# Kernel tuning notes

Measured on AMD Instinct MI355X. Metric: run time of the kernel, lower is better.

## Reference

```python
import jax, jax.numpy as jnp
import numpy as np
from jax import lax

# pywt db4 filters (8 taps)
_DEC_LO = np.array([-0.010597401784997278, 0.032883011666982945, 0.030841381835986965,
                    -0.18703481171888114, -0.02798376941698385, 0.6308807679295904,
                    0.7148465705525415, 0.23037781330885523])
_DEC_HI = np.array([-0.23037781330885523, 0.7148465705525415, -0.6308807679295904,
                    -0.02798376941698385, 0.18703481171888114, 0.030841381835986965,
                    -0.032883011666982945, -0.010597401784997278])
_REC_LO = _DEC_LO[::-1].copy()
_REC_HI = _DEC_HI[::-1].copy()
_L = 8  # filter length
LEVELS = 4


def _dwt_level(x):
    # x: (M, n) -> (cA, cD) each (M, (n+_L-1)//2), pywt 'symmetric' mode
    xe = jnp.pad(x, ((0, 0), (_L - 1, _L - 1)), mode='symmetric')[:, 1:]
    ker = jnp.stack([_DEC_LO[::-1], _DEC_HI[::-1]]).astype(x.dtype)[:, None, :]  # (2,1,L)
    y = lax.conv_general_dilated(xe[:, None, :], ker, (2,), 'VALID')  # (M,2,m)
    return y[:, 0], y[:, 1]


def _idwt_level(ca, cd, out_len):
    # inverse DWT, cropped to out_len (matches length of next-finer approximation)
    inp = jnp.stack([ca, cd], axis=1)  # (M,2,m)
    ker = jnp.stack([_REC_LO[::-1], _REC_HI[::-1]]).astype(ca.dtype)[None]  # (1,2,L)
    y = lax.conv_general_dilated(inp, ker, (1,), [(_L - 1, _L - 1)], lhs_dilation=(2,))
    return y[:, 0, _L - 2:_L - 2 + out_len]


def setup_inputs() -> dict:
    key = jax.random.key(0)
    k1, k2, k3, k4 = jax.random.split(key, 4)
    B, N, C = 32, 8192, 64
    m = N
    for _ in range(LEVELS):
        m = (m + _L - 1) // 2  # 518
    scale = 1.0 / (C * C)
    return {
        'x': jax.random.normal(k1, (B, N, C), jnp.float32),
        'w1': scale * jax.random.uniform(k2, (C, C, m), jnp.float32),
        'w2': scale * jax.random.uniform(k3, (C, C, m), jnp.float32),
        'dense_kernel': jax.random.normal(k4, (C, C), jnp.float32) / jnp.sqrt(C).astype(jnp.float32),
        'dense_bias': jnp.zeros((C,), jnp.float32),
    }


def reference(x, w1, w2, dense_kernel, dense_bias):
    B, N, C = x.shape
    xc = jnp.transpose(x, (0, 2, 1)).reshape(B * C, N)  # per-(batch,channel) signals
    # analysis: multi-level DWT
    lens, details = [], []
    a = xc
    for _ in range(LEVELS):
        lens.append(a.shape[1])
        a, d = _dwt_level(a)
        details.append(d)
    m = a.shape[1]
    # channel mixing on coarsest approximation and coarsest detail (WNO kernel)
    a = jnp.einsum('bim,iom->bom', a.reshape(B, C, m), w1).reshape(B * C, m)
    details[-1] = jnp.einsum('bim,iom->bom', details[-1].reshape(B, C, m), w2).reshape(B * C, m)
    # synthesis: multi-level IDWT
    for j in range(LEVELS - 1, -1, -1):
        a = _idwt_level(a, details[j], lens[j])
    y = jnp.transpose(a.reshape(B, C, N), (0, 2, 1))
    shortcut = x @ dense_kernel + dense_bias  # Dense 1x1 shortcut
    out = y + shortcut
    return out * jnp.tanh(jax.nn.softplus(out))  # mish
```

## Files before the change

kernel.cpp:

```cpp
#include <hip/hip_runtime.h>
#include <hip/hip_bf16.h>
#include <stdint.h>

typedef __attribute__((ext_vector_type(8))) short short8;
typedef __attribute__((ext_vector_type(4))) float floatx4;

__device__ __constant__ float c_DL[8] = {
    -0.010597401784997278f, 0.032883011666982945f, 0.030841381835986965f,
    -0.18703481171888114f, -0.02798376941698385f, 0.6308807679295904f,
    0.7148465705525415f, 0.23037781330885523f};
__device__ __constant__ float c_DH[8] = {
    -0.23037781330885523f, 0.7148465705525415f, -0.6308807679295904f,
    -0.02798376941698385f, 0.18703481171888114f, 0.030841381835986965f,
    -0.032883011666982945f, -0.010597401784997278f};
__device__ __constant__ float c_RL[8] = {
    0.23037781330885523f, 0.7148465705525415f, 0.6308807679295904f,
    -0.02798376941698385f, -0.18703481171888114f, 0.030841381835986965f,
    0.032883011666982945f, -0.010597401784997278f};
__device__ __constant__ float c_RH[8] = {
    -0.010597401784997278f, -0.032883011666982945f, 0.030841381835986965f,
    0.18703481171888114f, -0.02798376941698385f, -0.6308807679295904f,
    0.7148465705525415f, -0.23037781330885523f};

__device__ __forceinline__ float bflo(uint32_t u) { return __uint_as_float(u << 16); }
__device__ __forceinline__ float bfhi(uint32_t u) { return __uint_as_float(u & 0xffff0000u); }
__device__ __forceinline__ float bfu(unsigned short u) { return __uint_as_float(((uint32_t)u) << 16); }
__device__ __forceinline__ short f2bs(float f) {
  __hip_bfloat16 h = __float2bfloat16(f);
  return *reinterpret_cast<short*>(&h);
}

__device__ __forceinline__ int reflect_idx(int t, int n) {
  if (t < 0) t = -1 - t;
  if (t >= n) t = 2 * n - 1 - t;
  return t;
}

#define S1R 4100
#define S2R 2056

__global__ __launch_bounds__(256) void k_wT(const float* __restrict__ w1,
                                            const float* __restrict__ w2,
                                            float* __restrict__ wt1,
                                            float* __restrict__ wt2) {
  const float* w = blockIdx.z ? w2 : w1;
  float* wt = blockIdx.z ? wt2 : wt1;
  const int io0 = blockIdx.x * 64;
  const int p0 = blockIdx.y * 64;
  const int pw = min(64, 518 - p0);
  const int tid = threadIdx.x;
  __shared__ float ts[64 * 65];
  for (int idx = tid; idx < 64 * 64; idx += 256) {
    int row = idx >> 6, col = idx & 63;
    if (col < pw) ts[row * 65 + col] = w[(size_t)(io0 + row) * 518 + p0 + col];
  }
  __syncthreads();
  for (int idx = tid; idx < 64 * 64; idx += 256) {
    int pl = idx >> 6, io = idx & 63;
    if (pl < pw) wt[(size_t)(p0 + pl) * 4096 + io0 + io] = ts[io * 65 + pl];
  }
}

#define NT1 134
#define XTS 138
__global__ __launch_bounds__(256) void k_dwt_first(const float* __restrict__ x,
                                                   __hip_bfloat16* __restrict__ outa,
                                                   __hip_bfloat16* __restrict__ outd) {
  const int b = blockIdx.y;
  const int k0 = blockIdx.x * 64;
  const int tid = threadIdx.x;
  __shared__ float xs[64 * XTS];

  const float4* x4 = (const float4*)x;
  for (int idx = tid; idx < NT1 * 16; idx += 256) {
    int nl = idx >> 4, cq = idx & 15;
    int t = 2 * k0 - 6 + nl;
    int n = reflect_idx(t, 8192);
    float4 v = x4[((size_t)b * 8192 + n) * 16 + cq];
    xs[(4 * cq + 0) * XTS + nl] = v.x;
    xs[(4 * cq + 1) * XTS + nl] = v.y;
    xs[(4 * cq + 2) * XTS + nl] = v.z;
    xs[(4 * cq + 3) * XTS + nl] = v.w;
  }
  __syncthreads();

  const int kk = tid & 63;
  const int k = k0 + kk;
  if (k >= 4099) return;
  for (int c = (tid >> 6); c < 64; c += 4) {
    const float2* p = (const float2*)&xs[c * XTS + 2 * kk];
    float2 p0 = p[0], p1 = p[1], p2 = p[2], p3 = p[3];
    float lo = c_DL[0] * p3.y + c_DL[1] * p3.x + c_DL[2] * p2.y + c_DL[3] * p2.x +
               c_DL[4] * p1.y + c_DL[5] * p1.x + c_DL[6] * p0.y + c_DL[7] * p0.x;
    float hi = c_DH[0] * p3.y + c_DH[1] * p3.x + c_DH[2] * p2.y + c_DH[3] * p2.x +
               c_DH[4] * p1.y + c_DH[5] * p1.x + c_DH[6] * p0.y + c_DH[7] * p0.x;
    size_t s = (size_t)b * 64 + c;
    outa[s * S1R + k] = __float2bfloat16(lo);
    outd[s * S1R + k] = __float2bfloat16(hi);
  }
}

__global__ __launch_bounds__(256) void k_ana234(const __hip_bfloat16* __restrict__ a1,
                                                __hip_bfloat16* __restrict__ d2o,
                                                float* __restrict__ d3o,
                                                float* __restrict__ a4o,
                                                float* __restrict__ d4o) {
  const int bid = blockIdx.x;
  const int s = (bid & 7) * 256 + (bid >> 3);
  const int i_ch = s >> 5;
  const int bb = s & 31;
  const int r = bb * 64 + i_ch;
  const int tid = threadIdx.x;
  __shared__ float s1[4100];
  __shared__ float s2[2054];
  __shared__ float s3[1032];

  const uint2* row2 = (const uint2*)(a1 + (size_t)r * S1R);
  for (int i = tid; i < 1025; i += 256) {
    uint2 u = row2[i];
    int e = 4 * i;
    s1[e] = bflo(u.x); s1[e + 1] = bfhi(u.x);
    s1[e + 2] = bflo(u.y); s1[e + 3] = bfhi(u.y);
  }
  __syncthreads();

  for (int k = tid; k < 2053; k += 256) {
    float lo = 0.f, hi = 0.f;
    if (k >= 3 && k <= 2048) {
      const float2* p = (const float2*)&s1[2 * k - 6];
      float2 v0 = p[0], v1 = p[1], v2 = p[2], v3 = p[3];
      lo = c_RL[0]*v0.x + c_RL[1]*v0.y + c_RL[2]*v1.x + c_RL[3]*v1.y +
           c_RL[4]*v2.x + c_RL[5]*v2.y + c_RL[6]*v3.x + c_RL[7]*v3.y;
      hi = c_RH[0]*v0.x + c_RH[1]*v0.y + c_RH[2]*v1.x + c_RH[3]*v1.y +
           c_RH[4]*v2.x + c_RH[5]*v2.y + c_RH[6]*v3.x + c_RH[7]*v3.y;
    } else {
#pragma unroll
      for (int j = 0; j < 8; ++j) {
        float v = s1[reflect_idx(2 * k + 1 - j, 4099)];
        lo += c_DL[j] * v; hi += c_DH[j] * v;
      }
    }
    d2o[(size_t)r * S2R + k] = __float2bfloat16(hi);
    s2[k] = lo;
  }
  __syncthreads();

  for (int k = tid; k < 1030; k += 256) {
    float lo = 0.f, hi = 0.f;
    if (k >= 3 && k <= 1025) {
      const float2* p = (const float2*)&s2[2 * k - 6];
      float2 v0 = p[0], v1 = p[1], v2 = p[2], v3 = p[3];
      lo = c_RL[0]*v0.x + c_RL[1]*v0.y + c_RL[2]*v1.x + c_RL[3]*v1.y +
           c_RL[4]*v2.x + c_RL[5]*v2.y + c_RL[6]*v3.x + c_RL[7]*v3.y;
      hi = c_RH[0]*v0.x + c_RH[1]*v0.y + c_RH[2]*v1.x + c_RH[3]*v1.y +
           c_RH[4]*v2.x + c_RH[5]*v2.y + c_RH[6]*v3.x + c_RH[7]*v3.y;
    } else {
#pragma unroll
      for (int j = 0; j < 8; ++j) {
        float v = s2[reflect_idx(2 * k + 1 - j, 2053)];
        lo += c_DL[j] * v; hi += c_DH[j] * v;
      }
    }
    d3o[(size_t)r * 1030 + k] = hi;
    s3[k] = lo;
  }
  __syncthreads();

  for (int k = tid; k < 518; k += 256) {
    float lo = 0.f, hi = 0.f;
    if (k >= 3 && k <= 514) {
      const float2* p = (const float2*)&s3[2 * k - 6];
      float2 v0 = p[0], v1 = p[1], v2 = p[2], v3 = p[3];
      lo = c_RL[0]*v0.x + c_RL[1]*v0.y + c_RL[2]*v1.x + c_RL[3]*v1.y +
           c_RL[4]*v2.x + c_RL[5]*v2.y + c_RL[6]*v3.x + c_RL[7]*v3.y;
      hi = c_RH[0]*v0.x + c_RH[1]*v0.y + c_RH[2]*v1.x + c_RH[3]*v1.y +
           c_RH[4]*v2.x + c_RH[5]*v2.y + c_RH[6]*v3.x + c_RH[7]*v3.y;
    } else {
#pragma unroll
      for (int j = 0; j < 8; ++j) {
        float v = s3[reflect_idx(2 * k + 1 - j, 1030)];
        lo += c_DL[j] * v; hi += c_DH[j] * v;
      }
    }
    a4o[(size_t)k * 2048 + s] = lo;
    d4o[(size_t)k * 2048 + s] = hi;
  }
}

__global__ __launch_bounds__(256) void k_mix_pc(const float* __restrict__ wt1,
                                                const float* __restrict__ wt2,
                                                const float* __restrict__ a4t,
                                                const float* __restrict__ d4t,
                                                float* __restrict__ am,
                                                float* __restrict__ dm) {
  const int bx = blockIdx.x;
  const int xcd = bx & 7;
  const int j = bx >> 3;
  const int p = (xcd < 6) ? (xcd * 65 + j) : (390 + (xcd - 6) * 64 + j);

  const float* w = blockIdx.y ? wt2 : wt1;
  const float* act = blockIdx.y ? d4t : a4t;
  float* outp = blockIdx.y ? dm : am;

  __shared__ float ws[4096];
  __shared__ float as_[2048];
  const int tid = threadIdx.x;

  const float4* wg = (const float4*)(w + (size_t)p * 4096);
  const float4* ag = (const float4*)(act + (size_t)p * 2048);
  float4* ws4 = (float4*)ws;
  float4* as4 = (float4*)as_;
  for (int t = tid; t < 1024; t += 256) ws4[t] = wg[t];
  for (int t = tid; t < 512; t += 256) as4[t] = ag[t];
  __syncthreads();

  const int o0 = (tid & 15) * 4;
  const int bq = tid >> 4;
  floatx4 acc0 = {0.f, 0.f, 0.f, 0.f}, acc1 = {0.f, 0.f, 0.f, 0.f};

#pragma unroll 8
  for (int i = 0; i < 64; ++i) {
    floatx4 wv = *(const floatx4*)&ws[i * 64 + o0];
    float a0 = as_[i * 32 + bq];
    float a1 = as_[i * 32 + bq + 16];
#pragma unroll
    for (int q = 0; q < 4; ++q) {
      acc0[q] += a0 * wv[q];
      acc1[q] += a1 * wv[q];
    }
  }

#pragma unroll
  for (int q = 0; q < 4; ++q) {
    outp[(size_t)(bq * 64 + o0 + q) * 518 + p] = acc0[q];
    outp[(size_t)((bq + 16) * 64 + o0 + q) * 518 + p] = acc1[q];
  }
}

__global__ __launch_bounds__(256) void k_syn(const float* __restrict__ a4m,
                                             const float* __restrict__ d4m,
                                             const float* __restrict__ d3,
                                             const __hip_bfloat16* __restrict__ d2,
                                             __hip_bfloat16* __restrict__ r1out) {
  const int r = blockIdx.x;
  const int tid = threadIdx.x;
  __shared__ float sa[518], sd[518], s3d[1030], r3[1030], d2s[2056], r2[2053];
  for (int i = tid; i < 518; i += 256) {
    sa[i] = a4m[(size_t)r * 518 + i];
    sd[i] = d4m[(size_t)r * 518 + i];
  }
  for (int i = tid; i < 1030; i += 256) s3d[i] = d3[(size_t)r * 1030 + i];
  {
    const uint2* p2 = (const uint2*)(d2 + (size_t)r * S2R);
    for (int i = tid; i < 514; i += 256) {
      uint2 u = p2[i];
      int e = 4 * i;
      d2s[e] = bflo(u.x); d2s[e + 1] = bfhi(u.x);
      d2s[e + 2] = bflo(u.y); d2s[e + 3] = bfhi(u.y);
    }
  }
  __syncthreads();
  for (int s = tid; s < 1030; s += 256) {
    int u = s >> 1, par = s & 1;
    float acc = 0.f;
#pragma unroll
    for (int t = 0; t < 4; ++t) {
      int i = u + 3 - t;
      float fl = par ? c_RL[2 * t + 1] : c_RL[2 * t];
      float fh = par ? c_RH[2 * t + 1] : c_RH[2 * t];
      acc += fl * sa[i] + fh * sd[i];
    }
    r3[s] = acc;
  }
  __syncthreads();
  for (int s = tid; s < 2053; s += 256) {
    int u = s >> 1, par = s & 1;
    float acc = 0.f;
#pragma unroll
    for (int t = 0; t < 4; ++t) {
      int i = u + 3 - t;
      float fl = par ? c_RL[2 * t + 1] : c_RL[2 * t];
      float fh = par ? c_RH[2 * t + 1] : c_RH[2 * t];
      acc += fl * r3[i] + fh * s3d[i];
    }
    r2[s] = acc;
  }
  __syncthreads();
  for (int s = tid; s < 4099; s += 256) {
    int u = s >> 1, par = s & 1;
    float acc = 0.f;
#pragma unroll
    for (int t = 0; t < 4; ++t) {
      int i = u + 3 - t;
      float fl = par ? c_RL[2 * t + 1] : c_RL[2 * t];
      float fh = par ? c_RH[2 * t + 1] : c_RH[2 * t];
      acc += fl * r2[i] + fh * d2s[i];
    }
    r1out[(size_t)r * S1R + s] = __float2bfloat16(acc);
  }
}

#define RAS 68
__global__ __launch_bounds__(256) void k_epilogue(const __hip_bfloat16* __restrict__ r1,
                                                  const __hip_bfloat16* __restrict__ dd1,
                                                  const float* __restrict__ x,
                                                  const float* __restrict__ dk,
                                                  const float* __restrict__ bias,
                                                  float* __restrict__ out) {
  const int b = blockIdx.y;
  const int n0 = blockIdx.x * 64;
  const int u0 = n0 >> 1;
  const int tid = threadIdx.x;
  const int lane = tid & 63;
  const int w = tid >> 6;

  __shared__ __hip_bfloat16 Ktf[4096];
  __shared__ float ra[36 * RAS];
  __shared__ float rd[36 * RAS];

  {
    int o = tid & 63;
    int ot = o >> 4, m16 = o & 15;
    for (int it = 0; it < 2; ++it) {
      int slot = (tid >> 6) + 4 * it;
      int ks = slot >> 2, hi = slot & 3;
      int c0 = ks * 32 + hi * 8;
      short8 f;
#pragma unroll
      for (int kq2 = 0; kq2 < 8; ++kq2)
        f[kq2] = f2bs(dk[(size_t)(c0 + kq2) * 64 + o]);
      *(short8*)&Ktf[((ot * 2 + ks) * 64 + hi * 16 + m16) * 8] = f;
    }
  }
  {
    int o2 = tid >> 2;
    const ushort4* pr4 = (const ushort4*)(r1 + (size_t)(b * 64 + o2) * S1R + u0);
    const ushort4* pd4 = (const ushort4*)(dd1 + (size_t)(b * 64 + o2) * S1R + u0);
    for (int q = tid & 3; q < 9; q += 4) {
      ushort4 v = pr4[q];
      int i0 = 4 * q;
      ra[(i0 + 0) * RAS + o2] = bfu(v.x);
      ra[(i0 + 1) * RAS + o2] = bfu(v.y);
      ra[(i0 + 2) * RAS + o2] = bfu(v.z);
      ra[(i0 + 3) * RAS + o2] = bfu(v.w);
      ushort4 d = pd4[q];
      rd[(i0 + 0) * RAS + o2] = bfu(d.x);
      rd[(i0 + 1) * RAS + o2] = bfu(d.y);
      rd[(i0 + 2) * RAS + o2] = bfu(d.z);
      rd[(i0 + 3) * RAS + o2] = bfu(d.w);
    }
  }
  __syncthreads();

  const int m16 = lane & 15;
  const int kq = (lane >> 4) * 8;
  const int nrow = w * 16 + m16;
  const float* xrow = x + ((size_t)b * 8192 + n0 + nrow) * 64;

  floatx4 acc[4];
#pragma unroll
  for (int ot = 0; ot < 4; ++ot) acc[ot] = (floatx4){0.f, 0.f, 0.f, 0.f};

#pragma unroll
  for (int ks = 0; ks < 2; ++ks) {
    float4 xa = *(const float4*)(xrow + ks * 32 + kq);
    float4 xb = *(const float4*)(xrow + ks * 32 + kq + 4);
    short8 af;
    af[0] = f2bs(xa.x); af[1] = f2bs(xa.y); af[2] = f2bs(xa.z); af[3] = f2bs(xa.w);
    af[4] = f2bs(xb.x); af[5] = f2bs(xb.y); af[6] = f2bs(xb.z); af[7] = f2bs(xb.w);
#pragma unroll
    for (int ot = 0; ot < 4; ++ot) {
      short8 bf = *(const short8*)&Ktf[((ot * 2 + ks) * 64 + lane) * 8];
      acc[ot] = __builtin_amdgcn_mfma_f32_16x16x32_bf16(af, bf, acc[ot], 0, 0, 0);
    }
  }

  const int rbase = (lane >> 4) * 4;
#pragma unroll
  for (int ot = 0; ot < 4; ++ot) {
    int o_loc = ot * 16 + m16;
    float bo = bias[o_loc];
#pragma unroll
    for (int rg = 0; rg < 4; ++rg) {
      int n_loc = w * 16 + rbase + rg;
      int ul = n_loc >> 1, par = n_loc & 1;
      float wv = 0.f;
#pragma unroll
      for (int t = 0; t < 4; ++t) {
        int i = ul + 3 - t;
        float fl = par ? c_RL[2 * t + 1] : c_RL[2 * t];
        float fh = par ? c_RH[2 * t + 1] : c_RH[2 * t];
        wv += fl * ra[i * RAS + o_loc] + fh * rd[i * RAS + o_loc];
      }
      float v = acc[ot][rg] + wv + bo;
      float e = __expf(fminf(v, 15.f));
      float num = e * (e + 2.f);
      float mm = (v > 15.f) ? v : v * (num / (num + 2.f));
      __builtin_nontemporal_store(mm, &out[((size_t)b * 8192 + n0 + n_loc) * 64 + o_loc]);
    }
  }
}

extern "C" void kernel_launch(void* const* d_in, const int* in_sizes, int n_in,
                              void* d_out, int out_size, void* d_ws, size_t ws_size,
                              hipStream_t stream) {
  const float* x    = (const float*)d_in[0];
  const float* w1   = (const float*)d_in[1];
  const float* w2   = (const float*)d_in[2];
  const float* dk   = (const float*)d_in[3];
  const float* bias = (const float*)d_in[4];
  float* out = (float*)d_out;

  const size_t R = 2048;

  float* wf = (float*)d_ws;
  float* d3f = wf; wf += R * 1030;
  float* a4t = wf; wf += R * 518;
  float* d4t = wf; wf += R * 518;
  float* a4m = wf; wf += R * 518;
  float* d4m = wf; wf += R * 518;
  float* wt1 = wf; wf += (size_t)518 * 4096;
  float* wt2 = wf; wf += (size_t)518 * 4096;
  __hip_bfloat16* wb = (__hip_bfloat16*)wf;
  __hip_bfloat16* a1b = wb; wb += R * S1R;
  __hip_bfloat16* d1b = wb; wb += R * S1R;
  __hip_bfloat16* d2b = wb; wb += R * S2R;

  k_wT<<<dim3(64, 9, 2), 256, 0, stream>>>(w1, w2, wt1, wt2);
  k_dwt_first<<<dim3(65, 32), 256, 0, stream>>>(x, a1b, d1b);
  k_ana234<<<dim3(2048), 256, 0, stream>>>(a1b, d2b, d3f, a4t, d4t);
  k_mix_pc<<<dim3(518, 2), 256, 0, stream>>>(wt1, wt2, a4t, d4t, a4m, d4m);
  k_syn<<<dim3(2048), 256, 0, stream>>>(a4m, d4m, d3f, d2b, a1b);
  k_epilogue<<<dim3(128, 32), 256, 0, stream>>>(a1b, d1b, x, dk, bias, out);
}
```

Measured before the change: 249.0 us.

## Fuse synthesis levels 4-2 into epilogue kernel with per-tile halo recomputation

Removes the separate k_syn kernel and recomputes the inverse DWT levels 4, 3 and 2 inside each epilogue tile from the coarse coefficients, using a small halo window per 64-sample tile. This drops one kernel launch and the global round trip of the bf16 level-1 approximation (write then read). In exchange it adds redundant halo computation across tiles, extra shared memory (about 24KB more per block, which may lower occupancy) and more synchronisation barriers inside the epilogue.

```diff
diff --git a/kernel.cpp b/kernel.cpp
--- a/kernel.cpp
+++ b/kernel.cpp
@@ -237,90 +237,38 @@
   }
 }
 
-__global__ __launch_bounds__(256) void k_syn(const float* __restrict__ a4m,
-                                             const float* __restrict__ d4m,
-                                             const float* __restrict__ d3,
-                                             const __hip_bfloat16* __restrict__ d2,
-                                             __hip_bfloat16* __restrict__ r1out) {
-  const int r = blockIdx.x;
-  const int tid = threadIdx.x;
-  __shared__ float sa[518], sd[518], s3d[1030], r3[1030], d2s[2056], r2[2053];
-  for (int i = tid; i < 518; i += 256) {
-    sa[i] = a4m[(size_t)r * 518 + i];
-    sd[i] = d4m[(size_t)r * 518 + i];
-  }
-  for (int i = tid; i < 1030; i += 256) s3d[i] = d3[(size_t)r * 1030 + i];
-  {
-    const uint2* p2 = (const uint2*)(d2 + (size_t)r * S2R);
-    for (int i = tid; i < 514; i += 256) {
-      uint2 u = p2[i];
-      int e = 4 * i;
-      d2s[e] = bflo(u.x); d2s[e + 1] = bfhi(u.x);
-      d2s[e + 2] = bflo(u.y); d2s[e + 3] = bfhi(u.y);
-    }
-  }
-  __syncthreads();
-  for (int s = tid; s < 1030; s += 256) {
-    int u = s >> 1, par = s & 1;
-    float acc = 0.f;
-#pragma unroll
-    for (int t = 0; t < 4; ++t) {
-      int i = u + 3 - t;
-      float fl = par ? c_RL[2 * t + 1] : c_RL[2 * t];
-      float fh = par ? c_RH[2 * t + 1] : c_RH[2 * t];
-      acc += fl * sa[i] + fh * sd[i];
-    }
-    r3[s] = acc;
-  }
-  __syncthreads();
-  for (int s = tid; s < 2053; s += 256) {
-    int u = s >> 1, par = s & 1;
-    float acc = 0.f;
-#pragma unroll
-    for (int t = 0; t < 4; ++t) {
-      int i = u + 3 - t;
-      float fl = par ? c_RL[2 * t + 1] : c_RL[2 * t];
-      float fh = par ? c_RH[2 * t + 1] : c_RH[2 * t];
-      acc += fl * r3[i] + fh * s3d[i];
-    }
-    r2[s] = acc;
-  }
-  __syncthreads();
-  for (int s = tid; s < 4099; s += 256) {
-    int u = s >> 1, par = s & 1;
-    float acc = 0.f;
-#pragma unroll
-    for (int t = 0; t < 4; ++t) {
-      int i = u + 3 - t;
-      float fl = par ? c_RL[2 * t + 1] : c_RL[2 * t];
-      float fh = par ? c_RH[2 * t + 1] : c_RH[2 * t];
-      acc += fl * r2[i] + fh * d2s[i];
-    }
-    r1out[(size_t)r * S1R + s] = __float2bfloat16(acc);
-  }
-}
-
 #define RAS 68
-__global__ __launch_bounds__(256) void k_epilogue(const __hip_bfloat16* __restrict__ r1,
+__global__ __launch_bounds__(256) void k_epilogue(const float* __restrict__ a4m,
+                                                  const float* __restrict__ d4m,
+                                                  const float* __restrict__ d3,
+                                                  const __hip_bfloat16* __restrict__ d2,
                                                   const __hip_bfloat16* __restrict__ dd1,
                                                   const float* __restrict__ x,
                                                   const float* __restrict__ dk,
                                                   const float* __restrict__ bias,
                                                   float* __restrict__ out) {
   const int b = blockIdx.y;
-  const int n0 = blockIdx.x * 64;
+  const int bx = blockIdx.x;
+  const int n0 = bx * 64;
   const int u0 = n0 >> 1;
   const int tid = threadIdx.x;
   const int lane = tid & 63;
   const int w = tid >> 6;
 
   __shared__ __hip_bfloat16 Ktf[4096];
-  __shared__ float ra[36 * RAS];
-  __shared__ float rd[36 * RAS];
+  __shared__ float rds[36 * RAS];
+  __shared__ float ras[36 * RAS];
+  __shared__ float scr[6045];
+  float* sa4 = scr;
+  float* sd4 = scr + 650;
+  float* sd3 = scr + 1300;
+  float* sd2 = scr + 2210;
+  float* r3s = scr + 3770;
+  float* r2s = scr + 4680;
 
   {
     int o = tid & 63;
-    int ot = o >> 4, m16 = o & 15;
+    int ot = o >> 4, m16o = o & 15;
     for (int it = 0; it < 2; ++it) {
       int slot = (tid >> 6) + 4 * it;
       int ks = slot >> 2, hi = slot & 3;
@@ -329,26 +277,90 @@
 #pragma unroll
       for (int kq2 = 0; kq2 < 8; ++kq2)
         f[kq2] = f2bs(dk[(size_t)(c0 + kq2) * 64 + o]);
-      *(short8*)&Ktf[((ot * 2 + ks) * 64 + hi * 16 + m16) * 8] = f;
+      *(short8*)&Ktf[((ot * 2 + ks) * 64 + hi * 16 + m16o) * 8] = f;
     }
   }
   {
-    int o2 = tid >> 2;
-    const ushort4* pr4 = (const ushort4*)(r1 + (size_t)(b * 64 + o2) * S1R + u0);
-    const ushort4* pd4 = (const ushort4*)(dd1 + (size_t)(b * 64 + o2) * S1R + u0);
-    for (int q = tid & 3; q < 9; q += 4) {
-      ushort4 v = pr4[q];
-      int i0 = 4 * q;
-      ra[(i0 + 0) * RAS + o2] = bfu(v.x);
-      ra[(i0 + 1) * RAS + o2] = bfu(v.y);
-      ra[(i0 + 2) * RAS + o2] = bfu(v.z);
-      ra[(i0 + 3) * RAS + o2] = bfu(v.w);
-      ushort4 d = pd4[q];
-      rd[(i0 + 0) * RAS + o2] = bfu(d.x);
-      rd[(i0 + 1) * RAS + o2] = bfu(d.y);
-      rd[(i0 + 2) * RAS + o2] = bfu(d.z);
-      rd[(i0 + 3) * RAS + o2] = bfu(d.w);
-    }
+    const int o = tid & 63;
+    const int part = tid >> 6;
+    const size_t r = (size_t)b * 64 + o;
+    if (part == 0) {
+      const float2* pa = (const float2*)(a4m + r * 518 + bx * 4);
+      const float2* pd = (const float2*)(d4m + r * 518 + bx * 4);
+#pragma unroll
+      for (int q = 0; q < 5; ++q) {
+        float2 va = pa[q], vd = pd[q];
+        sa4[(2 * q + 0) * 65 + o] = va.x; sa4[(2 * q + 1) * 65 + o] = va.y;
+        sd4[(2 * q + 0) * 65 + o] = vd.x; sd4[(2 * q + 1) * 65 + o] = vd.y;
+      }
+    } else if (part == 1) {
+      const float2* p3 = (const float2*)(d3 + r * 1030 + bx * 8);
+#pragma unroll
+      for (int q = 0; q < 7; ++q) {
+        float2 v = p3[q];
+        sd3[(2 * q + 0) * 65 + o] = v.x; sd3[(2 * q + 1) * 65 + o] = v.y;
+      }
+    } else if (part == 2) {
+      const ushort4* p24 = (const ushort4*)(d2 + r * S2R + bx * 16);
+#pragma unroll
+      for (int q = 0; q < 6; ++q) {
+        ushort4 v = p24[q];
+        sd2[(4 * q + 0) * 65 + o] = bfu(v.x); sd2[(4 * q + 1) * 65 + o] = bfu(v.y);
+        sd2[(4 * q + 2) * 65 + o] = bfu(v.z); sd2[(4 * q + 3) * 65 + o] = bfu(v.w);
+      }
+    } else {
+      const ushort4* pd1 = (const ushort4*)(dd1 + r * S1R + u0);
+#pragma unroll
+      for (int q = 0; q < 9; ++q) {
+        ushort4 v = pd1[q];
+        int i0 = 4 * q;
+        rds[(i0 + 0) * RAS + o] = bfu(v.x); rds[(i0 + 1) * RAS + o] = bfu(v.y);
+        rds[(i0 + 2) * RAS + o] = bfu(v.z); rds[(i0 + 3) * RAS + o] = bfu(v.w);
+      }
+    }
+  }
+  __syncthreads();
+
+  for (int it = tid; it < 14 * 64; it += 256) {
+    int o = it & 63, wc = it >> 6;
+    int base = wc >> 1, par = wc & 1;
+    float acc = 0.f;
+#pragma unroll
+    for (int t = 0; t < 4; ++t) {
+      int i = base + 3 - t;
+      float fl = par ? c_RL[2 * t + 1] : c_RL[2 * t];
+      float fh = par ? c_RH[2 * t + 1] : c_RH[2 * t];
+      acc += fl * sa4[i * 65 + o] + fh * sd4[i * 65 + o];
+    }
+    r3s[wc * 65 + o] = acc;
+  }
+  __syncthreads();
+  for (int it = tid; it < 21 * 64; it += 256) {
+    int o = it & 63, vc = it >> 6;
+    int base = vc >> 1, par = vc & 1;
+    float acc = 0.f;
+#pragma unroll
+    for (int t = 0; t < 4; ++t) {
+      int i = base + 3 - t;
+      float fl = par ? c_RL[2 * t + 1] : c_RL[2 * t];
+      float fh = par ? c_RH[2 * t + 1] : c_RH[2 * t];
+      acc += fl * r3s[i * 65 + o] + fh * sd3[i * 65 + o];
+    }
+    r2s[vc * 65 + o] = acc;
+  }
+  __syncthreads();
+  for (int it = tid; it < 35 * 64; it += 256) {
+    int o = it & 63, uc = it >> 6;
+    int base = uc >> 1, par = uc & 1;
+    float acc = 0.f;
+#pragma unroll
+    for (int t = 0; t < 4; ++t) {
+      int i = base + 3 - t;
+      float fl = par ? c_RL[2 * t + 1] : c_RL[2 * t];
+      float fh = par ? c_RH[2 * t + 1] : c_RH[2 * t];
+      acc += fl * r2s[i * 65 + o] + fh * sd2[i * 65 + o];
+    }
+    ras[uc * RAS + o] = acc;
   }
   __syncthreads();
 
@@ -390,7 +402,7 @@
         int i = ul + 3 - t;
         float fl = par ? c_RL[2 * t + 1] : c_RL[2 * t];
         float fh = par ? c_RH[2 * t + 1] : c_RH[2 * t];
-        wv += fl * ra[i * RAS + o_loc] + fh * rd[i * RAS + o_loc];
+        wv += fl * ras[i * RAS + o_loc] + fh * rds[i * RAS + o_loc];
       }
       float v = acc[ot][rg] + wv + bo;
       float e = __expf(fminf(v, 15.f));
@@ -430,6 +442,5 @@
   k_dwt_first<<<dim3(65, 32), 256, 0, stream>>>(x, a1b, d1b);
   k_ana234<<<dim3(2048), 256, 0, stream>>>(a1b, d2b, d3f, a4t, d4t);
   k_mix_pc<<<dim3(518, 2), 256, 0, stream>>>(wt1, wt2, a4t, d4t, a4m, d4m);
-  k_syn<<<dim3(2048), 256, 0, stream>>>(a4m, d4m, d3f, d2b, a1b);
-  k_epilogue<<<dim3(128, 32), 256, 0, stream>>>(a1b, d1b, x, dk, bias, out);
-}
+  k_epilogue<<<dim3(128, 32), 256, 0, stream>>>(a4m, d4m, d3f, d2b, d1b, x, dk, bias, out);
+}
```

New measurement: 267.6 us. +7.4%, slower.
